# Kernel tuning notes

Measured on AMD Instinct MI355X. Metric: run time of the kernel, lower is better.

Reference implementation:

```python
import jax, jax.numpy as jnp
import numpy as np
from math import sqrt


def sparsemax(z):
    # z: [..., S]; sparsemax along last axis (Martins & Astudillo 2016)
    S = z.shape[-1]
    z_sorted = jnp.flip(jnp.sort(z, axis=-1), axis=-1)          # descending
    cssv = jnp.cumsum(z_sorted, axis=-1)                        # cumulative sums
    r = jnp.arange(1, S + 1, dtype=z.dtype)                     # 1..S
    support = z_sorted * r > (cssv - 1.0)                       # k in support
    k = jnp.sum(support, axis=-1, keepdims=True)                # support size >=1
    cssv_k = jnp.take_along_axis(cssv, k.astype(jnp.int32) - 1, axis=-1)
    tau = (cssv_k - 1.0) / k.astype(z.dtype)
    return jnp.maximum(z - tau, 0.0)


def setup_inputs() -> dict:
    key = jax.random.key(0)
    kq, kk, kv = jax.random.split(key, 3)
    B, H, S, D = 2, 12, 2048, 64
    return {
        "query": jax.random.normal(kq, (B, H, S, D), dtype=jnp.float32),
        "key": jax.random.normal(kk, (B, H, S, D), dtype=jnp.float32),
        "value": jax.random.normal(kv, (B, H, S, D), dtype=jnp.float32),
        "attention_mask": jnp.ones((B, S), dtype=jnp.float32),
        "attention_scale": jnp.zeros((H,), dtype=jnp.float32),
    }


def reference(query, key, value, attention_mask, attention_scale):
    B, H, S, D = query.shape
    neg = jnp.finfo(query.dtype).min
    add_mask = (1.0 - attention_mask[:, None, None, :]) * neg   # [B,1,1,S]
    scores = jnp.einsum("bhqd,bhkd->bhqk", query, key) / sqrt(D)
    scores = scores * jnp.exp(attention_scale)[None, :, None, None]
    scores = scores + add_mask
    probs = sparsemax(scores)                                   # [B,H,S,S]
    return jnp.einsum("bhqk,bhkd->bhqd", probs, value)
```

## Files before the change

### kernel.cpp

```cpp
#include <hip/hip_runtime.h>
#include <hip/hip_fp16.h>

constexpr int B = 2, H = 12, S = 2048, D = 64;
constexpr int TQ = 16;
constexpr int NBLK_Q = S / TQ;
constexpr size_t BHSD = (size_t)B * H * S * D;

using f16x8 = _Float16 __attribute__((ext_vector_type(8)));
using f16x4 = _Float16 __attribute__((ext_vector_type(4)));
using f32x4 = float   __attribute__((ext_vector_type(4)));

__device__ __forceinline__ int swz2(int q, int k) {
    return k ^ ((((k >> 6) ^ q) & 7) << 3);
}

__global__ __launch_bounds__(256)
void cvt_k_kernel(const float* __restrict__ K, _Float16* __restrict__ Kh) {
    const int bh   = blockIdx.x >> 6;
    const int t    = (blockIdx.x & 63) * 2 + (threadIdx.x >> 7);
    const int f    = threadIdx.x & 127;
    const int c2   = f >> 6, grp = (f >> 4) & 3, row = f & 15;
    const size_t bhSD = (size_t)bh * S * D;
    const float* src = K + bhSD + (size_t)(t * 16 + row) * D + c2 * 32 + grp * 8;
    const float4 x0 = *reinterpret_cast<const float4*>(src);
    const float4 x1 = *reinterpret_cast<const float4*>(src + 4);
    f16x8 y;
    y[0] = (_Float16)x0.x; y[1] = (_Float16)x0.y; y[2] = (_Float16)x0.z; y[3] = (_Float16)x0.w;
    y[4] = (_Float16)x1.x; y[5] = (_Float16)x1.y; y[6] = (_Float16)x1.z; y[7] = (_Float16)x1.w;
    *reinterpret_cast<f16x8*>(Kh + bhSD + (size_t)t * 1024 + f * 8) = y;
}

__global__ __launch_bounds__(256)
void tr_v_kernel(const float* __restrict__ V, _Float16* __restrict__ Vt) {
    const int bh = blockIdx.x >> 6;
    const int c  = blockIdx.x & 63;
    const int f  = threadIdx.x;
    const int dh = f >> 7, n2 = (f >> 6) & 1, grp = (f >> 4) & 3, row = f & 15;
    const int d  = dh * 32 + n2 * 16 + row;
    const size_t bhSD = (size_t)bh * S * D;
    const float* src = V + bhSD + (size_t)(c * 32 + grp * 8) * D + d;
    f16x8 y;
    #pragma unroll
    for (int e = 0; e < 8; ++e) y[e] = (_Float16)src[e * D];
    *reinterpret_cast<f16x8*>(Vt + bhSD + (size_t)c * 2048 + f * 8) = y;
}

template <bool PRE>
__global__ __launch_bounds__(1024, 8)
void sparsemax_attn_kernel(const float* __restrict__ Q, const float* __restrict__ K,
                           const float* __restrict__ V, const float* __restrict__ mask,
                           const float* __restrict__ scale, float* __restrict__ out,
                           const _Float16* __restrict__ Kh, const _Float16* __restrict__ Vt)
{
    __shared__ alignas(16) _Float16 s_sh[TQ * 2048];
    __shared__ alignas(16) float    madd_sh[S];
    __shared__ float tau_s[TQ];

    const int tid  = threadIdx.x;
    const int lane = tid & 63;
    const int w    = tid >> 6;
    const int row  = lane & 15;
    const int grp  = lane >> 4;
    const int bh   = blockIdx.x / NBLK_Q;
    const int qt   = blockIdx.x - bh * NBLK_Q;
    const int b    = bh / H;
    const int h    = bh - b * H;
    const int q0   = qt * TQ;

    const size_t bhSD = (size_t)bh * S * D;
    const float* mrow = mask + (size_t)b * S;
    const float  sc   = __expf(scale[h]) * 0.125f;

    madd_sh[tid]        = (1.0f - mrow[tid])        * -1.0e9f;
    madd_sh[tid + 1024] = (1.0f - mrow[tid + 1024]) * -1.0e9f;

    f16x8 qa[2];
    {
        const float* qr = Q + bhSD + (size_t)(q0 + row) * D + grp * 8;
        #pragma unroll
        for (int c = 0; c < 2; ++c) {
            const float4 x0 = *reinterpret_cast<const float4*>(qr + c * 32);
            const float4 x1 = *reinterpret_cast<const float4*>(qr + c * 32 + 4);
            qa[c][0] = (_Float16)(x0.x * sc); qa[c][1] = (_Float16)(x0.y * sc);
            qa[c][2] = (_Float16)(x0.z * sc); qa[c][3] = (_Float16)(x0.w * sc);
            qa[c][4] = (_Float16)(x1.x * sc); qa[c][5] = (_Float16)(x1.y * sc);
            qa[c][6] = (_Float16)(x1.z * sc); qa[c][7] = (_Float16)(x1.w * sc);
        }
    }
    __syncthreads();

    if constexpr (PRE) {
        const _Float16* ksrc = Kh + bhSD + (size_t)(w * 8) * 1024 + lane * 8;
        f16x8 ka0 = *reinterpret_cast<const f16x8*>(ksrc);
        f16x8 ka1 = *reinterpret_cast<const f16x8*>(ksrc + 512);
        #pragma unroll
        for (int i = 0; i < 8; ++i) {
            f16x8 nb0, nb1;
            if (i < 7) {
                nb0 = *reinterpret_cast<const f16x8*>(ksrc + (i + 1) * 1024);
                nb1 = *reinterpret_cast<const f16x8*>(ksrc + (i + 1) * 1024 + 512);
            }
            f32x4 acc = {0.f, 0.f, 0.f, 0.f};
            acc = __builtin_amdgcn_mfma_f32_16x16x32_f16(ka0, qa[0], acc, 0, 0, 0);
            acc = __builtin_amdgcn_mfma_f32_16x16x32_f16(ka1, qa[1], acc, 0, 0, 0);
            const int key0 = (w * 8 + i) * 16;
            const float4 ma = *reinterpret_cast<const float4*>(madd_sh + key0 + grp * 4);
            f16x4 st;
            #pragma unroll
            for (int r = 0; r < 4; ++r) {
                const float v = fminf(fmaxf(acc[r] + (&ma.x)[r], -60000.0f), 60000.0f);
                st[r] = (_Float16)v;
            }
            *reinterpret_cast<f16x4*>(&s_sh[row * 2048 + swz2(row, key0 + grp * 4)]) = st;
            ka0 = nb0; ka1 = nb1;
        }
    } else {
        for (int t = w * 8; t < w * 8 + 8; ++t) {
            const int key0 = t * 16;
            const float* kp = K + bhSD + (size_t)(key0 + row) * D + grp * 8;
            f16x8 kb0, kb1;
            #pragma unroll
            for (int c = 0; c < 2; ++c) {
                const float4 x0 = *reinterpret_cast<const float4*>(kp + c * 32);
                const float4 x1 = *reinterpret_cast<const float4*>(kp + c * 32 + 4);
                f16x8& kb = c ? kb1 : kb0;
                kb[0] = (_Float16)x0.x; kb[1] = (_Float16)x0.y;
                kb[2] = (_Float16)x0.z; kb[3] = (_Float16)x0.w;
                kb[4] = (_Float16)x1.x; kb[5] = (_Float16)x1.y;
                kb[6] = (_Float16)x1.z; kb[7] = (_Float16)x1.w;
            }
            f32x4 acc = {0.f, 0.f, 0.f, 0.f};
            acc = __builtin_amdgcn_mfma_f32_16x16x32_f16(kb0, qa[0], acc, 0, 0, 0);
            acc = __builtin_amdgcn_mfma_f32_16x16x32_f16(kb1, qa[1], acc, 0, 0, 0);
            const float4 ma = *reinterpret_cast<const float4*>(madd_sh + key0 + grp * 4);
            f16x4 st;
            #pragma unroll
            for (int r = 0; r < 4; ++r) {
                const float v = fminf(fmaxf(acc[r] + (&ma.x)[r], -60000.0f), 60000.0f);
                st[r] = (_Float16)v;
            }
            *reinterpret_cast<f16x4*>(&s_sh[row * 2048 + swz2(row, key0 + grp * 4)]) = st;
        }
    }
    __syncthreads();

    {
        const _Float16* zrow = &s_sh[w * 2048];
        float z32[32];
        #pragma unroll
        for (int j = 0; j < 4; ++j) {
            const f16x8 zv = *reinterpret_cast<const f16x8*>(&zrow[swz2(w, lane * 32 + j * 8)]);
            #pragma unroll
            for (int e = 0; e < 8; ++e) z32[j * 8 + e] = (float)zv[e];
        }
        float m = z32[0];
        #pragma unroll
        for (int j = 1; j < 32; ++j) m = fmaxf(m, z32[j]);
        #pragma unroll
        for (int off = 32; off >= 1; off >>= 1) m = fmaxf(m, __shfl_xor(m, off));
        const float thr = m - 1.0f;
        float c0 = -1.0e30f, c1 = -1.0e30f, c2 = -1.0e30f;
        int lc = 0;
        #pragma unroll
        for (int j = 0; j < 32; ++j) {
            const float zz = z32[j];
            if (zz > thr) {
                c2 = (lc == 2) ? zz : c2;
                c1 = (lc == 1) ? zz : c1;
                c0 = (lc == 0) ? zz : c0;
                ++lc;
            }
        }
        float tau = thr;
        if (__ballot(lc > 3) == 0ULL) {
            #pragma unroll 1
            for (int it = 0; it < 24; ++it) {
                const float d0 = c0 - tau, d1 = c1 - tau, d2 = c2 - tau;
                float s = fmaxf(d0, 0.f) + fmaxf(d1, 0.f) + fmaxf(d2, 0.f);
                float c = (d0 > 0.f ? 1.f : 0.f) + (d1 > 0.f ? 1.f : 0.f) + (d2 > 0.f ? 1.f : 0.f);
                #pragma unroll
                for (int off = 32; off >= 1; off >>= 1) {
                    s += __shfl_xor(s, off);
                    c += __shfl_xor(c, off);
                }
                const float tn = tau + (s - 1.0f) / c;
                if (!(tn > tau)) break;
                tau = tn;
            }
        } else {
            #pragma unroll 1
            for (int it = 0; it < 32; ++it) {
                float s = 0.f, c = 0.f;
                #pragma unroll
                for (int j = 0; j < 32; ++j) {
                    const float d = z32[j] - tau;
                    s += fmaxf(d, 0.f);
                    c += (d > 0.f ? 1.f : 0.f);
                }
                #pragma unroll
                for (int off = 32; off >= 1; off >>= 1) {
                    s += __shfl_xor(s, off);
                    c += __shfl_xor(c, off);
                }
                const float tn = tau + (s - 1.0f) / c;
                if (!(tn > tau)) break;
                tau = tn;
            }
        }
        if (lane == 0) tau_s[w] = tau;
    }
    __syncthreads();

    const float tau_row = tau_s[row];
    f16x8 t8;
    {
        const _Float16 th = (_Float16)tau_row;
        #pragma unroll
        for (int e = 0; e < 8; ++e) t8[e] = th;
    }
    f32x4 o[4] = {{0.f,0.f,0.f,0.f},{0.f,0.f,0.f,0.f},{0.f,0.f,0.f,0.f},{0.f,0.f,0.f,0.f}};
    if constexpr (PRE) {
        const _Float16* vsrc = Vt + bhSD + (size_t)w * 8192 + lane * 8;
        f16x8 va0 = *reinterpret_cast<const f16x8*>(vsrc);
        f16x8 va1 = *reinterpret_cast<const f16x8*>(vsrc + 512);
        #pragma unroll
        for (int hc = 0; hc < 8; ++hc) {
            f16x8 nb0, nb1;
            if (hc < 7) {
                nb0 = *reinterpret_cast<const f16x8*>(vsrc + (hc + 1) * 1024);
                nb1 = *reinterpret_cast<const f16x8*>(vsrc + (hc + 1) * 1024 + 512);
            }
            f16x8 pa;
            if ((hc & 1) == 0) {
                const int k0 = (w * 4 + (hc >> 1)) * 32;
                const f16x8 zv = *reinterpret_cast<const f16x8*>(
                    &s_sh[row * 2048 + swz2(row, k0 + grp * 8)]);
                pa = __builtin_elementwise_max(zv - t8, (f16x8)(_Float16)0.0f);
            } else {
                const int k0 = (w * 4 + (hc >> 1)) * 32;
                const f16x8 zv = *reinterpret_cast<const f16x8*>(
                    &s_sh[row * 2048 + swz2(row, k0 + grp * 8)]);
                pa = __builtin_elementwise_max(zv - t8, (f16x8)(_Float16)0.0f);
            }
            const int nb = (hc & 1) * 2;
            o[nb]     = __builtin_amdgcn_mfma_f32_16x16x32_f16(pa, va0, o[nb],     0, 0, 0);
            o[nb + 1] = __builtin_amdgcn_mfma_f32_16x16x32_f16(pa, va1, o[nb + 1], 0, 0, 0);
            va0 = nb0; va1 = nb1;
        }
    } else {
        for (int c = w * 4; c < w * 4 + 4; ++c) {
            const int k0 = c * 32;
            const f16x8 zv = *reinterpret_cast<const f16x8*>(
                &s_sh[row * 2048 + swz2(row, k0 + grp * 8)]);
            const f16x8 pa2 = __builtin_elementwise_max(zv - t8, (f16x8)(_Float16)0.0f);
            #pragma unroll
            for (int n = 0; n < 4; ++n) {
                f16x8 vb;
                #pragma unroll
                for (int j = 0; j < 8; ++j)
                    vb[j] = (_Float16)V[bhSD + (size_t)(k0 + grp * 8 + j) * D + n * 16 + row];
                o[n] = __builtin_amdgcn_mfma_f32_16x16x32_f16(pa2, vb, o[n], 0, 0, 0);
            }
        }
    }
    __syncthreads();

    float* red = reinterpret_cast<float*>(s_sh);
    #pragma unroll
    for (int n = 0; n < 4; ++n)
        #pragma unroll
        for (int r = 0; r < 4; ++r)
            red[w * 1024 + (grp * 4 + r) * 64 + n * 16 + row] = o[n][r];
    __syncthreads();

    {
        const int q = tid >> 6;
        const int d = tid & 63;
        float sum = 0.f;
        #pragma unroll
        for (int p = 0; p < 16; ++p)
            sum += red[p * 1024 + q * 64 + d];
        out[bhSD + (size_t)(q0 + q) * D + d] = sum;
    }
}

extern "C" void kernel_launch(void* const* d_in, const int* in_sizes, int n_in,
                              void* d_out, int out_size, void* d_ws, size_t ws_size,
                              hipStream_t stream) {
    const float* Q     = (const float*)d_in[0];
    const float* K     = (const float*)d_in[1];
    const float* V     = (const float*)d_in[2];
    const float* mask  = (const float*)d_in[3];
    const float* scale = (const float*)d_in[4];
    float* out = (float*)d_out;

    const size_t need = 2 * BHSD * sizeof(_Float16);
    if (ws_size >= need) {
        _Float16* Kh = (_Float16*)d_ws;
        _Float16* Vt = Kh + BHSD;
        cvt_k_kernel<<<dim3(B * H * 64), dim3(256), 0, stream>>>(K, Kh);
        tr_v_kernel<<<dim3(B * H * 64), dim3(256), 0, stream>>>(V, Vt);
        sparsemax_attn_kernel<true><<<dim3(B * H * NBLK_Q), dim3(1024), 0, stream>>>(
            Q, K, V, mask, scale, out, Kh, Vt);
    } else {
        sparsemax_attn_kernel<false><<<dim3(B * H * NBLK_Q), dim3(1024), 0, stream>>>(
            Q, K, V, mask, scale, out, nullptr, nullptr);
    }
}
```

Measured before the change: 145.7 us.

## Reduce partial outputs via LDS atomics, keep scores in f16, restructure PV loop

Replaces the cross-wave output reduction through s_sh, which needed a barrier plus 16 strided reads per output, with float atomicAdd into a small padded LDS buffer that is zeroed at kernel start. The sparsemax pass now keeps scores as packed f16 vectors, taking the max with vector f16 max and converting per element only when needed. This cuts register pressure from the 32-float array. The PV loop drops software prefetching of V in favour of four straight loads per 32-key chunk, and the upper clamp on scores is removed. Ordering of the LDS float atomics is nondeterministic, and without the upper clamp large scores could overflow f16.

```diff
diff --git a/kernel.cpp b/kernel.cpp
--- a/kernel.cpp
+++ b/kernel.cpp
@@ -54,6 +54,7 @@
 {
     __shared__ alignas(16) _Float16 s_sh[TQ * 2048];
     __shared__ alignas(16) float    madd_sh[S];
+    __shared__ alignas(16) float    red_sh[TQ][68];
     __shared__ float tau_s[TQ];
 
     const int tid  = threadIdx.x;
@@ -73,6 +74,8 @@
 
     madd_sh[tid]        = (1.0f - mrow[tid])        * -1.0e9f;
     madd_sh[tid + 1024] = (1.0f - mrow[tid + 1024]) * -1.0e9f;
+    reinterpret_cast<float*>(red_sh)[tid] = 0.0f;
+    if (tid < TQ * 68 - 1024) reinterpret_cast<float*>(red_sh)[1024 + tid] = 0.0f;
 
     f16x8 qa[2];
     {
@@ -107,10 +110,8 @@
             const float4 ma = *reinterpret_cast<const float4*>(madd_sh + key0 + grp * 4);
             f16x4 st;
             #pragma unroll
-            for (int r = 0; r < 4; ++r) {
-                const float v = fminf(fmaxf(acc[r] + (&ma.x)[r], -60000.0f), 60000.0f);
-                st[r] = (_Float16)v;
-            }
+            for (int r = 0; r < 4; ++r)
+                st[r] = (_Float16)fmaxf(acc[r] + (&ma.x)[r], -60000.0f);
             *reinterpret_cast<f16x4*>(&s_sh[row * 2048 + swz2(row, key0 + grp * 4)]) = st;
             ka0 = nb0; ka1 = nb1;
         }
@@ -135,10 +136,8 @@
             const float4 ma = *reinterpret_cast<const float4*>(madd_sh + key0 + grp * 4);
             f16x4 st;
             #pragma unroll
-            for (int r = 0; r < 4; ++r) {
-                const float v = fminf(fmaxf(acc[r] + (&ma.x)[r], -60000.0f), 60000.0f);
-                st[r] = (_Float16)v;
-            }
+            for (int r = 0; r < 4; ++r)
+                st[r] = (_Float16)fmaxf(acc[r] + (&ma.x)[r], -60000.0f);
             *reinterpret_cast<f16x4*>(&s_sh[row * 2048 + swz2(row, key0 + grp * 4)]) = st;
         }
     }
@@ -146,31 +145,29 @@
 
     {
         const _Float16* zrow = &s_sh[w * 2048];
-        float z32[32];
-        #pragma unroll
-        for (int j = 0; j < 4; ++j) {
-            const f16x8 zv = *reinterpret_cast<const f16x8*>(&zrow[swz2(w, lane * 32 + j * 8)]);
-            #pragma unroll
-            for (int e = 0; e < 8; ++e) z32[j * 8 + e] = (float)zv[e];
-        }
-        float m = z32[0];
-        #pragma unroll
-        for (int j = 1; j < 32; ++j) m = fmaxf(m, z32[j]);
+        const f16x8 zv0 = *reinterpret_cast<const f16x8*>(&zrow[swz2(w, lane * 32 +  0)]);
+        const f16x8 zv1 = *reinterpret_cast<const f16x8*>(&zrow[swz2(w, lane * 32 +  8)]);
+        const f16x8 zv2 = *reinterpret_cast<const f16x8*>(&zrow[swz2(w, lane * 32 + 16)]);
+        const f16x8 zv3 = *reinterpret_cast<const f16x8*>(&zrow[swz2(w, lane * 32 + 24)]);
+        const f16x8 m8 = __builtin_elementwise_max(__builtin_elementwise_max(zv0, zv1),
+                                                   __builtin_elementwise_max(zv2, zv3));
+        float m = (float)m8[0];
+        #pragma unroll
+        for (int e = 1; e < 8; ++e) m = fmaxf(m, (float)m8[e]);
         #pragma unroll
         for (int off = 32; off >= 1; off >>= 1) m = fmaxf(m, __shfl_xor(m, off));
         const float thr = m - 1.0f;
         float c0 = -1.0e30f, c1 = -1.0e30f, c2 = -1.0e30f;
         int lc = 0;
-        #pragma unroll
-        for (int j = 0; j < 32; ++j) {
-            const float zz = z32[j];
-            if (zz > thr) {
-                c2 = (lc == 2) ? zz : c2;
-                c1 = (lc == 1) ? zz : c1;
-                c0 = (lc == 0) ? zz : c0;
-                ++lc;
-            }
-        }
+#define EXTRACT8(ZV) { _Pragma("unroll") for (int e = 0; e < 8; ++e) { \
+            const float zz = (float)(ZV)[e]; \
+            if (zz > thr) { \
+                c2 = (lc == 2) ? zz : c2; \
+                c1 = (lc == 1) ? zz : c1; \
+                c0 = (lc == 0) ? zz : c0; \
+                ++lc; } } }
+        EXTRACT8(zv0) EXTRACT8(zv1) EXTRACT8(zv2) EXTRACT8(zv3)
+#undef EXTRACT8
         float tau = thr;
         if (__ballot(lc > 3) == 0ULL) {
             #pragma unroll 1
@@ -191,12 +188,11 @@
             #pragma unroll 1
             for (int it = 0; it < 32; ++it) {
                 float s = 0.f, c = 0.f;
-                #pragma unroll
-                for (int j = 0; j < 32; ++j) {
-                    const float d = z32[j] - tau;
-                    s += fmaxf(d, 0.f);
-                    c += (d > 0.f ? 1.f : 0.f);
-                }
+#define ACC8(ZV) { _Pragma("unroll") for (int e = 0; e < 8; ++e) { \
+                const float d = (float)(ZV)[e] - tau; \
+                s += fmaxf(d, 0.f); c += (d > 0.f ? 1.f : 0.f); } }
+                ACC8(zv0) ACC8(zv1) ACC8(zv2) ACC8(zv3)
+#undef ACC8
                 #pragma unroll
                 for (int off = 32; off >= 1; off >>= 1) {
                     s += __shfl_xor(s, off);
@@ -221,31 +217,20 @@
     f32x4 o[4] = {{0.f,0.f,0.f,0.f},{0.f,0.f,0.f,0.f},{0.f,0.f,0.f,0.f},{0.f,0.f,0.f,0.f}};
     if constexpr (PRE) {
         const _Float16* vsrc = Vt + bhSD + (size_t)w * 8192 + lane * 8;
-        f16x8 va0 = *reinterpret_cast<const f16x8*>(vsrc);
-        f16x8 va1 = *reinterpret_cast<const f16x8*>(vsrc + 512);
-        #pragma unroll
-        for (int hc = 0; hc < 8; ++hc) {
-            f16x8 nb0, nb1;
-            if (hc < 7) {
-                nb0 = *reinterpret_cast<const f16x8*>(vsrc + (hc + 1) * 1024);
-                nb1 = *reinterpret_cast<const f16x8*>(vsrc + (hc + 1) * 1024 + 512);
-            }
-            f16x8 pa;
-            if ((hc & 1) == 0) {
-                const int k0 = (w * 4 + (hc >> 1)) * 32;
-                const f16x8 zv = *reinterpret_cast<const f16x8*>(
-                    &s_sh[row * 2048 + swz2(row, k0 + grp * 8)]);
-                pa = __builtin_elementwise_max(zv - t8, (f16x8)(_Float16)0.0f);
-            } else {
-                const int k0 = (w * 4 + (hc >> 1)) * 32;
-                const f16x8 zv = *reinterpret_cast<const f16x8*>(
-                    &s_sh[row * 2048 + swz2(row, k0 + grp * 8)]);
-                pa = __builtin_elementwise_max(zv - t8, (f16x8)(_Float16)0.0f);
-            }
-            const int nb = (hc & 1) * 2;
-            o[nb]     = __builtin_amdgcn_mfma_f32_16x16x32_f16(pa, va0, o[nb],     0, 0, 0);
-            o[nb + 1] = __builtin_amdgcn_mfma_f32_16x16x32_f16(pa, va1, o[nb + 1], 0, 0, 0);
-            va0 = nb0; va1 = nb1;
+        #pragma unroll
+        for (int cl = 0; cl < 4; ++cl) {
+            const int k0 = (w * 4 + cl) * 32;
+            const f16x8 zv = *reinterpret_cast<const f16x8*>(
+                &s_sh[row * 2048 + swz2(row, k0 + grp * 8)]);
+            const f16x8 pa = __builtin_elementwise_max(zv - t8, (f16x8)(_Float16)0.0f);
+            const f16x8 va0 = *reinterpret_cast<const f16x8*>(vsrc + cl * 2048);
+            const f16x8 va1 = *reinterpret_cast<const f16x8*>(vsrc + cl * 2048 + 512);
+            o[0] = __builtin_amdgcn_mfma_f32_16x16x32_f16(pa, va0, o[0], 0, 0, 0);
+            o[1] = __builtin_amdgcn_mfma_f32_16x16x32_f16(pa, va1, o[1], 0, 0, 0);
+            const f16x8 va2 = *reinterpret_cast<const f16x8*>(vsrc + cl * 2048 + 1024);
+            const f16x8 va3 = *reinterpret_cast<const f16x8*>(vsrc + cl * 2048 + 1536);
+            o[2] = __builtin_amdgcn_mfma_f32_16x16x32_f16(pa, va2, o[2], 0, 0, 0);
+            o[3] = __builtin_amdgcn_mfma_f32_16x16x32_f16(pa, va3, o[3], 0, 0, 0);
         }
     } else {
         for (int c = w * 4; c < w * 4 + 4; ++c) {
@@ -263,24 +248,18 @@
             }
         }
     }
-    __syncthreads();
-
-    float* red = reinterpret_cast<float*>(s_sh);
+
     #pragma unroll
     for (int n = 0; n < 4; ++n)
         #pragma unroll
         for (int r = 0; r < 4; ++r)
-            red[w * 1024 + (grp * 4 + r) * 64 + n * 16 + row] = o[n][r];
+            atomicAdd(&red_sh[grp * 4 + r][n * 16 + row], o[n][r]);
     __syncthreads();
 
     {
         const int q = tid >> 6;
         const int d = tid & 63;
-        float sum = 0.f;
-        #pragma unroll
-        for (int p = 0; p < 16; ++p)
-            sum += red[p * 1024 + q * 64 + d];
-        out[bhSD + (size_t)(q0 + q) * D + d] = sum;
+        out[bhSD + (size_t)(q0 + q) * D + d] = red_sh[q][d];
     }
 }
 
```

Result: slower. 391.6 us (+168.8%).
